# Kernel optimization log

Measured on AMD Instinct MI355X. Metric: run time of the kernel, lower is better.

## Reference

```python
import jax, jax.numpy as jnp
import numpy as np

N, D, NC, K = 4096, 64, 1000, 8192
ALPHA, BETA, GAMMA, SUPT = 0.02, 1.0, 1.0, 1.0
TEMP, BASE_TEMP = 0.05, 0.05
L_INTRA, L_IMEAN, L_IMIN, L_FISHER, EPS = 1.0, 0.1, 0.05, 0.1, 1e-6


def _l2norm(x, axis):
    # torch F.normalize: x / max(||x||, 1e-12)
    n = jnp.sqrt(jnp.sum(x * x, axis=axis, keepdims=True))
    return x / jnp.maximum(n, 1e-12)


def setup_inputs() -> dict:
    key = jax.random.key(0)
    k1, k2, k3, k4, k5 = jax.random.split(key, 5)
    # long-tailed class counts -> log_prior and class_weight buffers
    cls_arr = np.maximum((1280.0 * 0.01 ** (np.arange(NC) / (NC - 1))).astype(np.float32), 1.0)
    prior = cls_arr / cls_arr.sum()
    log_prior = jnp.asarray(np.log(prior), dtype=jnp.float32)
    inv = 1.0 / cls_arr
    class_weight = jnp.asarray((inv / inv.sum() * NC).astype(np.float32))
    feats = jax.random.normal(k1, (N, D), jnp.float32)
    logits = jax.random.normal(k2, (N, NC), jnp.float32)
    labels = jax.random.randint(k3, (N,), 0, NC)
    C = jax.random.normal(k4, (D, NC), jnp.float32) * 0.01  # learnable centers
    queue = jax.random.normal(k5, (K, D), jnp.float32)       # momentum queue buffer
    return {"feats": feats, "logits": logits, "labels": labels, "C": C,
            "queue": queue, "log_prior": log_prior, "class_weight": class_weight}


def reference(feats, logits, labels, C, queue, log_prior, class_weight):
    sg = jax.lax.stop_gradient
    # ---- weighted cross entropy on prior-adjusted logits ----
    sup_logits = (logits + log_prior) / SUPT
    logp = jax.nn.log_softmax(sup_logits, axis=1)
    w = class_weight[labels]
    nll = -jnp.take_along_axis(logp, labels[:, None], axis=1)[:, 0]
    ce_loss = jnp.sum(w * nll) / jnp.sum(w)

    # ---- normalize feats, enqueue (ptr=0, N<=K -> queue[:N] = feats) ----
    f = _l2norm(feats, axis=1)                       # [N, D]
    q = queue.at[:N].set(sg(f))                      # updated queue [K, D]
    centers = _l2norm(C, axis=0).T                   # [NC, D]

    neg_center_sim = f @ centers.T                   # [N, NC]
    neg_queue_sim = f @ q.T                          # [N, K]
    anchor_dot = jnp.concatenate([sg(sup_logits), neg_center_sim, neg_queue_sim], axis=1) / TEMP

    onehot = jax.nn.one_hot(labels, NC, dtype=jnp.float32)  # mask_sup == mask_cent
    mask = jnp.concatenate([onehot * BETA, onehot * ALPHA, jnp.zeros((N, K), jnp.float32)], axis=1)
    logits_mask = jnp.concatenate([jnp.ones((N, 2 * NC), jnp.float32),
                                   jnp.full((N, K), GAMMA, jnp.float32)], axis=1)

    anchor_dot = anchor_dot - sg(jnp.max(anchor_dot, axis=1, keepdims=True))
    exp_logits = jnp.exp(anchor_dot) * logits_mask
    log_prob = anchor_dot - jnp.log(jnp.sum(exp_logits, axis=1, keepdims=True) + 1e-12)
    mean_log_prob_pos = jnp.sum(mask * log_prob, axis=1) / (jnp.sum(mask, axis=1) + 1e-12)
    contrast_loss = -jnp.mean(mean_log_prob_pos) * (TEMP / BASE_TEMP)

    # ---- center regularizers ----
    gram = centers @ centers.T                       # centers are unit-norm rows
    sq = jnp.maximum(2.0 - 2.0 * gram, 1e-12)
    eye = jnp.eye(NC, dtype=bool)
    dist = jnp.sqrt(jnp.where(eye, 1e12, sq))
    dist_no_dg = jnp.where(eye, 1e6, dist)
    inter_min = jnp.min(dist_no_dg)
    inter_mean = jnp.sum(jnp.where(eye, 0.0, dist)) / (NC * (NC - 1))

    diff = f - centers[labels]                       # [N, D]
    intra_d = jnp.mean(jnp.sum(diff * diff, axis=1))
    mu_g = jnp.mean(f, axis=0, keepdims=True)
    cls_cnt = jnp.zeros((NC,), jnp.float32).at[labels].add(1.0)
    S_W = jnp.sum(diff * diff)
    S_B = jnp.sum(jnp.sum((centers - mu_g) ** 2, axis=1) * cls_cnt)
    fisher = S_B / (S_W + EPS)
    reg = (L_INTRA * intra_d + L_IMEAN / (inter_mean + EPS)
           + L_IMIN / (inter_min + EPS) + L_FISHER / (fisher + EPS))
    return ce_loss + contrast_loss + reg
```

## Files before the change

### kernel.cpp

```cpp
#include <hip/hip_runtime.h>
#include <math.h>

#define N_ 4096
#define D_ 64
#define NC_ 1000
#define KQ_ 8192
#define VCOLS 9192
#define VPAD  9216
#define PCH   73
#define TEMP_INV 20.0f
#define M0 20.25f
#define LOG2E 1.4426950408889634f
#define K2L  (TEMP_INV * LOG2E)
#define M0L  (M0 * LOG2E)

#define WS_F     0
#define WS_CENT  (WS_F + N_*D_)
#define WS_SUPM  (WS_CENT + NC_*D_)
#define WS_PSUP  (WS_SUPM + N_)
#define WS_PCENT (WS_PSUP + N_)
#define WS_CEPN  (WS_PCENT + N_)
#define WS_CEPD  (WS_CEPN + 1024)
#define WS_CSP   (WS_CEPD + 1024)
#define WS_GS    (WS_CSP + 16)
#define WS_GM    (WS_GS + 128)
#define WS_VF    (WS_GM + 128)
#define WS_VC    (WS_VF + 4096)
#define WS_TP    (WS_VC + 4096)
#define WS_CTR   (WS_TP + 64)
#define WS_PS    (WS_CTR + 4)
#define WS_BBF   (WS_PS + N_*PCH)

#define K1_BLOCKS 3082
#define K2_BLOCKS 4800
#define K3_BLOCKS 16

typedef __attribute__((ext_vector_type(8))) short short8_t;
typedef __attribute__((ext_vector_type(4))) float f32x4;

__device__ __forceinline__ ushort f2bf(float x) {
    union { float f; unsigned u; } v; v.f = x;
    unsigned r = (v.u + 0x7FFFu + ((v.u >> 16) & 1u)) >> 16;
    return (ushort)r;
}

__global__ __launch_bounds__(256) void k1(const float* __restrict__ feats,
                                          const float* __restrict__ C,
                                          const float* __restrict__ queue,
                                          const float* __restrict__ logits,
                                          const int* __restrict__ labels,
                                          const float* __restrict__ log_prior,
                                          const float* __restrict__ class_weight,
                                          float* __restrict__ ws,
                                          ushort* __restrict__ B) {
    int b = blockIdx.x;
    int t = threadIdx.x;
    if (b == 0 && t == 0) ((unsigned*)ws)[WS_CTR] = 0u;
    if (b < 1024) {
        int row  = b * 4 + (t >> 6);
        int lane = t & 63;
        float x = feats[row * D_ + lane];
        float ss = x * x;
        #pragma unroll
        for (int m = 32; m >= 1; m >>= 1) ss += __shfl_xor(ss, m, 64);
        float y = x / fmaxf(sqrtf(ss), 1e-12f);
        ws[WS_F + row * D_ + lane] = y;
        B[(size_t)(NC_ + row) * D_ + lane] = f2bf(y);
    } else if (b < 1028) {
        int c = (b - 1024) * 256 + t;
        if (c >= NC_) return;
        float v[D_];
        float ss = 0.0f;
        #pragma unroll
        for (int d = 0; d < D_; ++d) { float x = C[d * NC_ + c]; v[d] = x; ss += x * x; }
        float inv = 1.0f / fmaxf(sqrtf(ss), 1e-12f);
        #pragma unroll
        for (int d = 0; d < D_; ++d) {
            float y = v[d] * inv;
            ws[WS_CENT + c * D_ + d] = y;
            B[(size_t)c * D_ + d] = f2bf(y);
        }
    } else if (b < 2058) {
        int q = (b - 1028) * 256 + t;
        if (q >= (KQ_ - N_ + 24) * D_) return;
        int r = q >> 6, d = q & 63;
        ushort o = 0;
        if (r < KQ_ - N_) o = f2bf(queue[(size_t)(N_ + r) * D_ + d]);
        B[(size_t)(NC_ + N_ + r) * D_ + d] = o;
    } else {
        __shared__ float lp[1024];
        __shared__ float cep[4][2];
        int sid = b - 2058;
        if (t < 250) ((float4*)lp)[t] = ((const float4*)log_prior)[t];
        __syncthreads();
        int w = t >> 6, l = t & 63;
        int row = sid * 4 + w;
        const float* lrow = logits + (size_t)row * NC_;
        const float4* lrow4 = (const float4*)lrow;
        float vals[16];
        float m = -1e30f;
        #pragma unroll
        for (int it = 0; it < 4; ++it) {
            int idx = it * 64 + l;
            float4 v4 = (idx < 250) ? lrow4[idx]
                                    : make_float4(-1e30f, -1e30f, -1e30f, -1e30f);
            float4 p4 = (idx < 250) ? ((const float4*)lp)[idx]
                                    : make_float4(0, 0, 0, 0);
            vals[it * 4 + 0] = v4.x + p4.x;
            vals[it * 4 + 1] = v4.y + p4.y;
            vals[it * 4 + 2] = v4.z + p4.z;
            vals[it * 4 + 3] = v4.w + p4.w;
            #pragma unroll
            for (int k = 0; k < 4; ++k) m = fmaxf(m, vals[it * 4 + k]);
        }
        #pragma unroll
        for (int msk = 1; msk < 64; msk <<= 1) m = fmaxf(m, __shfl_xor(m, msk, 64));
        float s1 = 0.0f, s20 = 0.0f;
        #pragma unroll
        for (int k = 0; k < 16; ++k) {
            float d = vals[k] - m;
            s1  += __builtin_amdgcn_exp2f(d * LOG2E);
            s20 += __builtin_amdgcn_exp2f(d * K2L);
        }
        #pragma unroll
        for (int msk = 1; msk < 64; msk <<= 1) {
            s1  += __shfl_xor(s1, msk, 64);
            s20 += __shfl_xor(s20, msk, 64);
        }
        if (l == 0) {
            int lab = labels[row];
            float vpos = lrow[lab] + lp[lab];
            float wt = class_weight[lab];
            cep[w][0] = wt * (m + __logf(s1) - vpos);
            cep[w][1] = wt;
            ws[WS_SUPM + row] = TEMP_INV * m;
            ws[WS_PS + (size_t)row * PCH + (PCH - 1)] = s20;
            ws[WS_PSUP + row] = TEMP_INV * vpos;
        }
        __syncthreads();
        if (t == 0) {
            ws[WS_CEPN + sid] = cep[0][0] + cep[1][0] + cep[2][0] + cep[3][0];
            ws[WS_CEPD + sid] = cep[0][1] + cep[1][1] + cep[2][1] + cep[3][1];
        }
    }
}

__global__ __launch_bounds__(256) void k2(const ushort* __restrict__ B,
                                          const int* __restrict__ labels,
                                          const float* __restrict__ f,
                                          const float* __restrict__ cent,
                                          float* __restrict__ ws) {
    __shared__ ushort At[64 * 64];
    __shared__ ushort Bt[128 * 64];
    __shared__ float ssum[64][2];
    __shared__ float gs4[4], gm4[4];
    __shared__ float svf[4][64], svc[4][64], stp[4];

    int t = threadIdx.x;
    int l = t & 63, w = t >> 6;
    int bid = blockIdx.x;
    int wm = w >> 1, wn = w & 1;
    int lr = l & 15, lg = l >> 4;
    int lk = lg * 8;

    if (bid >= 192) {
        int g = bid - 192;
        int cg = g >> 6;
        int bx = g & 63;
        int r0 = bx * 64;
        int c0 = cg * 128;

        const ushort* Ag = B + (size_t)(NC_ + r0) * D_;
        const ushort* Bg = B + (size_t)c0 * D_;
        #pragma unroll
        for (int i = 0; i < 2; ++i) {
            int cid = t + i * 256;
            *(short8_t*)(At + cid * 8) = *(const short8_t*)(Ag + cid * 8);
        }
        #pragma unroll
        for (int i = 0; i < 4; ++i) {
            int cid = t + i * 256;
            *(short8_t*)(Bt + cid * 8) = *(const short8_t*)(Bg + cid * 8);
        }
        __syncthreads();

        short8_t a[2][2], bfr[4][2];
        #pragma unroll
        for (int rf = 0; rf < 2; ++rf) {
            int row = wm * 32 + rf * 16 + lr;
            #pragma unroll
            for (int ks = 0; ks < 2; ++ks)
                a[rf][ks] = *(const short8_t*)(At + row * D_ + lk + ks * 32);
        }
        #pragma unroll
        for (int cf = 0; cf < 4; ++cf) {
            int col = wn * 64 + cf * 16 + lr;
            #pragma unroll
            for (int ks = 0; ks < 2; ++ks)
                bfr[cf][ks] = *(const short8_t*)(Bt + col * D_ + lk + ks * 32);
        }

        f32x4 acc[2][4] = {};
        #pragma unroll
        for (int ks = 0; ks < 2; ++ks)
            #pragma unroll
            for (int rf = 0; rf < 2; ++rf)
                #pragma unroll
                for (int cf = 0; cf < 4; ++cf)
                    acc[rf][cf] = __builtin_amdgcn_mfma_f32_16x16x32_bf16(
                        a[rf][ks], bfr[cf][ks], acc[rf][cf], 0, 0, 0);

        if (c0 < NC_) {
            #pragma unroll
            for (int rf = 0; rf < 2; ++rf)
                #pragma unroll
                for (int reg = 0; reg < 4; ++reg) {
                    int row = r0 + wm * 32 + rf * 16 + lg * 4 + reg;
                    int lab = labels[row];
                    #pragma unroll
                    for (int cf = 0; cf < 4; ++cf) {
                        int col = c0 + wn * 64 + cf * 16 + lr;
                        if (col == lab) ws[WS_PCENT + row] = acc[rf][cf][reg];
                    }
                }
        }

        #pragma unroll
        for (int rf = 0; rf < 2; ++rf) {
            float se[4] = {0, 0, 0, 0};
            #pragma unroll
            for (int cf = 0; cf < 4; ++cf)
                #pragma unroll
                for (int reg = 0; reg < 4; ++reg)
                    se[reg] += __builtin_amdgcn_exp2f(
                        fmaf(acc[rf][cf][reg], K2L, -M0L));
            #pragma unroll
            for (int reg = 0; reg < 4; ++reg) {
                float v = se[reg];
                #pragma unroll
                for (int msk = 1; msk < 16; msk <<= 1)
                    v += __shfl_xor(v, msk, 64);
                if (lr == 0) ssum[wm * 32 + rf * 16 + lg * 4 + reg][wn] = v;
            }
        }
        __syncthreads();
        if (t < 64)
            ws[WS_PS + (size_t)(r0 + t) * PCH + cg] = ssum[t][0] + ssum[t][1];
    } else if (bid < 128) {
        int g = bid;
        int gr = g >> 3, gc = g & 7;
        int r0 = gr * 64 + wm * 32;
        int c0 = gc * 128 + wn * 64;

        const ushort* Af = B + (size_t)(r0 + lr) * D_ + lk;
        const ushort* Bf = B + (size_t)(c0 + lr) * D_ + lk;

        short8_t a[2][2], bfr[4][2];
        #pragma unroll
        for (int rf = 0; rf < 2; ++rf)
            #pragma unroll
            for (int ks = 0; ks < 2; ++ks)
                a[rf][ks] = *(const short8_t*)(Af + rf * 16 * D_ + ks * 32);
        #pragma unroll
        for (int cf = 0; cf < 4; ++cf)
            #pragma unroll
            for (int ks = 0; ks < 2; ++ks)
                bfr[cf][ks] = *(const short8_t*)(Bf + cf * 16 * D_ + ks * 32);

        f32x4 acc[2][4] = {};
        #pragma unroll
        for (int ks = 0; ks < 2; ++ks)
            #pragma unroll
            for (int rf = 0; rf < 2; ++rf)
                #pragma unroll
                for (int cf = 0; cf < 4; ++cf)
                    acc[rf][cf] = __builtin_amdgcn_mfma_f32_16x16x32_bf16(
                        a[rf][ks], bfr[cf][ks], acc[rf][cf], 0, 0, 0);

        float lsum = 0.0f, lmin = 1e30f;
        #pragma unroll
        for (int rf = 0; rf < 2; ++rf)
            #pragma unroll
            for (int cf = 0; cf < 4; ++cf)
                #pragma unroll
                for (int reg = 0; reg < 4; ++reg) {
                    int gi = r0 + rf * 16 + lg * 4 + reg;
                    int gj = c0 + cf * 16 + lr;
                    if (gi < NC_ && gj < NC_ && gi != gj) {
                        float d = sqrtf(fmaxf(2.0f - 2.0f * acc[rf][cf][reg], 1e-12f));
                        lsum += d;
                        lmin = fminf(lmin, d);
                    }
                }
        #pragma unroll
        for (int msk = 1; msk < 64; msk <<= 1) {
            lsum += __shfl_xor(lsum, msk, 64);
            lmin = fminf(lmin, __shfl_xor(lmin, msk, 64));
        }
        if (l == 0) { gs4[w] = lsum; gm4[w] = lmin; }
        __syncthreads();
        if (t == 0) {
            ws[WS_GS + g] = gs4[0] + gs4[1] + gs4[2] + gs4[3];
            ws[WS_GM + g] = fminf(fminf(gm4[0], gm4[1]), fminf(gm4[2], gm4[3]));
        }
    } else {
        int sb = bid - 128;
        int wid = sb * 4 + w;
        float vf = 0.0f, vc = 0.0f, tacc = 0.0f;
        for (int i = wid; i < N_; i += 256) {
            float x = f[i * D_ + l];
            float c = cent[labels[i] * D_ + l];
            vf += x; vc += c; tacc += x * c;
        }
        #pragma unroll
        for (int msk = 32; msk >= 1; msk >>= 1) tacc += __shfl_xor(tacc, msk, 64);
        svf[w][l] = vf; svc[w][l] = vc;
        if (l == 0) stp[w] = tacc;
        __syncthreads();
        if (w == 0) {
            ws[WS_VF + sb * 64 + l] = svf[0][l] + svf[1][l] + svf[2][l] + svf[3][l];
            ws[WS_VC + sb * 64 + l] = svc[0][l] + svc[1][l] + svc[2][l] + svc[3][l];
            if (l == 0) ws[WS_TP + sb] = stp[0] + stp[1] + stp[2] + stp[3];
        }
    }
}

__global__ __launch_bounds__(256) void k3(float* __restrict__ ws,
                                          float* __restrict__ out) {
    int t = threadIdx.x;
    int w = t >> 6, l = t & 63;
    int bid = blockIdx.x;
    __shared__ unsigned done;
    __shared__ float cb[4];

    {
        int row = bid * 256 + t;
        const float* pv = ws + WS_PS + (size_t)row * PCH;
        float s = 0.0f;
        #pragma unroll
        for (int c = 0; c < PCH - 1; ++c) s += pv[c];
        float msup = ws[WS_SUPM + row];
        float ssup = pv[PCH - 1];
        float M = fmaxf(M0, msup);
        float stot = s * __builtin_amdgcn_exp2f((M0 - M) * LOG2E)
                   + ssup * __builtin_amdgcn_exp2f((msup - M) * LOG2E);
        float logS = __logf(stot + 1e-12f);
        float lp1 = ws[WS_PSUP + row] - M - logS;
        float lp2 = ws[WS_PCENT + row] * TEMP_INV - M - logS;
        float cacc = (lp1 + 0.02f * lp2) / (1.02f + 1e-12f);
        #pragma unroll
        for (int msk = 1; msk < 64; msk <<= 1) cacc += __shfl_xor(cacc, msk, 64);
        if (l == 0) cb[w] = cacc;
        __syncthreads();
        if (t == 0) ws[WS_CSP + bid] = cb[0] + cb[1] + cb[2] + cb[3];
    }

    __threadfence();
    if (t == 0) done = atomicAdd((unsigned*)ws + WS_CTR, 1u);
    __syncthreads();
    if (done != K3_BLOCKS - 1) return;
    __threadfence();

    float csum = (t < 16) ? ws[WS_CSP + t] : 0.0f;
    float cen = 0.0f, ced = 0.0f;
    #pragma unroll
    for (int k = 0; k < 4; ++k) {
        cen += ws[WS_CEPN + t + k * 256];
        ced += ws[WS_CEPD + t + k * 256];
    }
    float gsum = 0, gmin = 1e30f, vf = 0, vc = 0, tp = 0;
    if (t < 64) {
        tp = ws[WS_TP + t];
        #pragma unroll 8
        for (int b = 0; b < 64; ++b) {
            vf += ws[WS_VF + b * 64 + t];
            vc += ws[WS_VC + b * 64 + t];
        }
    }
    if (t < 128) { gsum = ws[WS_GS + t]; gmin = ws[WS_GM + t]; }
    float mu_d = vf * (1.0f / (float)N_);
    float vmu  = vc * mu_d;
    float mumu = mu_d * mu_d;
    #pragma unroll
    for (int m = 32; m >= 1; m >>= 1) {
        csum += __shfl_xor(csum, m, 64);
        cen  += __shfl_xor(cen, m, 64);
        ced  += __shfl_xor(ced, m, 64);
        gsum += __shfl_xor(gsum, m, 64);
        gmin = fminf(gmin, __shfl_xor(gmin, m, 64));
        vmu  += __shfl_xor(vmu, m, 64);
        mumu += __shfl_xor(mumu, m, 64);
        tp   += __shfl_xor(tp, m, 64);
    }
    __shared__ float red[4][8];
    if (l == 0) {
        red[w][0] = csum; red[w][1] = cen; red[w][2] = ced; red[w][3] = gsum;
        red[w][4] = gmin; red[w][5] = vmu; red[w][6] = mumu; red[w][7] = tp;
    }
    __syncthreads();
    if (t == 0) {
        float CSM = red[0][0] + red[1][0] + red[2][0] + red[3][0];
        float CEN = red[0][1] + red[1][1] + red[2][1] + red[3][1];
        float CED = red[0][2] + red[1][2] + red[2][2] + red[3][2];
        float GSM = red[0][3] + red[1][3] + red[2][3] + red[3][3];
        float GMN = fminf(fminf(red[0][4], red[1][4]), fminf(red[2][4], red[3][4]));
        float VMU = red[0][5] + red[1][5] + red[2][5] + red[3][5];
        float MUMU = red[0][6] + red[1][6] + red[2][6] + red[3][6];
        float T   = red[0][7] + red[1][7] + red[2][7] + red[3][7];
        float SW = 2.0f * (float)N_ - 2.0f * T;
        float SB = (float)N_ - 2.0f * VMU + (float)N_ * MUMU;
        float intra = SW / (float)N_;
        float fisher = SB / (SW + 1e-6f);
        float ce = CEN / CED;
        float contrast = -(CSM / (float)N_);
        float inter_mean = GSM / (float)(NC_ * (NC_ - 1));
        float reg = intra + 0.1f / (inter_mean + 1e-6f)
                  + 0.05f / (GMN + 1e-6f) + 0.1f / (fisher + 1e-6f);
        out[0] = ce + contrast + reg;
    }
}

extern "C" void kernel_launch(void* const* d_in, const int* in_sizes, int n_in,
                              void* d_out, int out_size, void* d_ws, size_t ws_size,
                              hipStream_t stream) {
    const float* feats        = (const float*)d_in[0];
    const float* logits       = (const float*)d_in[1];
    const int*   labels       = (const int*)d_in[2];
    const float* C            = (const float*)d_in[3];
    const float* queue        = (const float*)d_in[4];
    const float* log_prior    = (const float*)d_in[5];
    const float* class_weight = (const float*)d_in[6];
    float* ws  = (float*)d_ws;
    float* out = (float*)d_out;
    ushort* Bbf = (ushort*)(ws + WS_BBF);

    hipLaunchKernelGGL(k1, dim3(K1_BLOCKS), dim3(256), 0, stream,
                       feats, C, queue, logits, labels, log_prior, class_weight,
                       ws, Bbf);
    hipLaunchKernelGGL(k2, dim3(K2_BLOCKS), dim3(256), 0, stream,
                       Bbf, labels, ws + WS_F, ws + WS_CENT, ws);
    hipLaunchKernelGGL(k3, dim3(K3_BLOCKS), dim3(256), 0, stream, ws, out);
}
```

Before: 46.26 us.

## Move CE row-softmax into GEMM kernel and swizzle LDS tiles

```diff
diff --git a/kernel.cpp b/kernel.cpp
--- a/kernel.cpp
+++ b/kernel.cpp
@@ -31,8 +31,8 @@
 #define WS_PS    (WS_CTR + 4)
 #define WS_BBF   (WS_PS + N_*PCH)
 
-#define K1_BLOCKS 3082
-#define K2_BLOCKS 4800
+#define K1_BLOCKS 2058
+#define K2_BLOCKS 5824
 #define K3_BLOCKS 16
 
 typedef __attribute__((ext_vector_type(8))) short short8_t;
@@ -44,13 +44,13 @@
     return (ushort)r;
 }
 
+__device__ __forceinline__ int swz(int byte) {
+    return byte ^ (((byte >> 7) & 7) << 4);
+}
+
 __global__ __launch_bounds__(256) void k1(const float* __restrict__ feats,
                                           const float* __restrict__ C,
                                           const float* __restrict__ queue,
-                                          const float* __restrict__ logits,
-                                          const int* __restrict__ labels,
-                                          const float* __restrict__ log_prior,
-                                          const float* __restrict__ class_weight,
                                           float* __restrict__ ws,
                                           ushort* __restrict__ B) {
     int b = blockIdx.x;
@@ -80,21 +80,125 @@
             ws[WS_CENT + c * D_ + d] = y;
             B[(size_t)c * D_ + d] = f2bf(y);
         }
-    } else if (b < 2058) {
+    } else {
         int q = (b - 1028) * 256 + t;
         if (q >= (KQ_ - N_ + 24) * D_) return;
         int r = q >> 6, d = q & 63;
         ushort o = 0;
         if (r < KQ_ - N_) o = f2bf(queue[(size_t)(N_ + r) * D_ + d]);
         B[(size_t)(NC_ + N_ + r) * D_ + d] = o;
-    } else {
-        __shared__ float lp[1024];
-        __shared__ float cep[4][2];
-        int sid = b - 2058;
+    }
+}
+
+__global__ __launch_bounds__(256) void k2(const ushort* __restrict__ B,
+                                          const float* __restrict__ logits,
+                                          const int* __restrict__ labels,
+                                          const float* __restrict__ log_prior,
+                                          const float* __restrict__ class_weight,
+                                          const float* __restrict__ f,
+                                          const float* __restrict__ cent,
+                                          float* __restrict__ ws) {
+    __shared__ char smem[25600];
+    int t = threadIdx.x;
+    int l = t & 63, w = t >> 6;
+    int bid = blockIdx.x;
+    int wm = w >> 1, wn = w & 1;
+    int lr = l & 15, lg = l >> 4;
+    int lk = lg * 8;
+
+    if (bid >= 1216) {
+        char* AtC = smem;
+        char* BtC = smem + 8192;
+        float (*ssum)[2] = (float(*)[2])(smem + 24576);
+
+        int g = bid - 1216;
+        int cg = g >> 6;
+        int bx = g & 63;
+        int r0 = bx * 64;
+        int c0 = cg * 128;
+
+        const short8_t* Ag8 = (const short8_t*)(B + (size_t)(NC_ + r0) * D_);
+        const short8_t* Bg8 = (const short8_t*)(B + (size_t)c0 * D_);
+        #pragma unroll
+        for (int i = 0; i < 2; ++i) {
+            int cid = t + i * 256;
+            *(short8_t*)(AtC + swz(cid * 16)) = Ag8[cid];
+        }
+        #pragma unroll
+        for (int i = 0; i < 4; ++i) {
+            int cid = t + i * 256;
+            *(short8_t*)(BtC + swz(cid * 16)) = Bg8[cid];
+        }
+        __syncthreads();
+
+        short8_t a[2][2], bfr[4][2];
+        #pragma unroll
+        for (int rf = 0; rf < 2; ++rf) {
+            int row = wm * 32 + rf * 16 + lr;
+            #pragma unroll
+            for (int ks = 0; ks < 2; ++ks)
+                a[rf][ks] = *(const short8_t*)(AtC + swz(row * 128 + ks * 64 + lg * 16));
+        }
+        #pragma unroll
+        for (int cf = 0; cf < 4; ++cf) {
+            int col = wn * 64 + cf * 16 + lr;
+            #pragma unroll
+            for (int ks = 0; ks < 2; ++ks)
+                bfr[cf][ks] = *(const short8_t*)(BtC + swz(col * 128 + ks * 64 + lg * 16));
+        }
+
+        f32x4 acc[2][4] = {};
+        #pragma unroll
+        for (int ks = 0; ks < 2; ++ks)
+            #pragma unroll
+            for (int rf = 0; rf < 2; ++rf)
+                #pragma unroll
+                for (int cf = 0; cf < 4; ++cf)
+                    acc[rf][cf] = __builtin_amdgcn_mfma_f32_16x16x32_bf16(
+                        a[rf][ks], bfr[cf][ks], acc[rf][cf], 0, 0, 0);
+
+        if (c0 < NC_) {
+            #pragma unroll
+            for (int rf = 0; rf < 2; ++rf)
+                #pragma unroll
+                for (int reg = 0; reg < 4; ++reg) {
+                    int row = r0 + wm * 32 + rf * 16 + lg * 4 + reg;
+                    int lab = labels[row];
+                    #pragma unroll
+                    for (int cf = 0; cf < 4; ++cf) {
+                        int col = c0 + wn * 64 + cf * 16 + lr;
+                        if (col == lab) ws[WS_PCENT + row] = acc[rf][cf][reg];
+                    }
+                }
+        }
+
+        #pragma unroll
+        for (int rf = 0; rf < 2; ++rf) {
+            float se[4] = {0, 0, 0, 0};
+            #pragma unroll
+            for (int cf = 0; cf < 4; ++cf)
+                #pragma unroll
+                for (int reg = 0; reg < 4; ++reg)
+                    se[reg] += __builtin_amdgcn_exp2f(
+                        fmaf(acc[rf][cf][reg], K2L, -M0L));
+            #pragma unroll
+            for (int reg = 0; reg < 4; ++reg) {
+                float v = se[reg];
+                #pragma unroll
+                for (int msk = 1; msk < 16; msk <<= 1)
+                    v += __shfl_xor(v, msk, 64);
+                if (lr == 0) ssum[wm * 32 + rf * 16 + lg * 4 + reg][wn] = v;
+            }
+        }
+        __syncthreads();
+        if (t < 64)
+            ws[WS_PS + (size_t)(r0 + t) * PCH + cg] = ssum[t][0] + ssum[t][1];
+    } else if (bid < 1024) {
+        float* lp = (float*)smem;
+        float (*cep)[2] = (float(*)[2])(smem + 4096);
         if (t < 250) ((float4*)lp)[t] = ((const float4*)log_prior)[t];
         __syncthreads();
-        int w = t >> 6, l = t & 63;
-        int row = sid * 4 + w;
+        int row = bid * 4 + w;
         const float* lrow = logits + (size_t)row * NC_;
         const float4* lrow4 = (const float4*)lrow;
         float vals[16];
@@ -139,115 +243,13 @@
         }
         __syncthreads();
         if (t == 0) {
-            ws[WS_CEPN + sid] = cep[0][0] + cep[1][0] + cep[2][0] + cep[3][0];
-            ws[WS_CEPD + sid] = cep[0][1] + cep[1][1] + cep[2][1] + cep[3][1];
-        }
-    }
-}
-
-__global__ __launch_bounds__(256) void k2(const ushort* __restrict__ B,
-                                          const int* __restrict__ labels,
-                                          const float* __restrict__ f,
-                                          const float* __restrict__ cent,
-                                          float* __restrict__ ws) {
-    __shared__ ushort At[64 * 64];
-    __shared__ ushort Bt[128 * 64];
-    __shared__ float ssum[64][2];
-    __shared__ float gs4[4], gm4[4];
-    __shared__ float svf[4][64], svc[4][64], stp[4];
-
-    int t = threadIdx.x;
-    int l = t & 63, w = t >> 6;
-    int bid = blockIdx.x;
-    int wm = w >> 1, wn = w & 1;
-    int lr = l & 15, lg = l >> 4;
-    int lk = lg * 8;
-
-    if (bid >= 192) {
-        int g = bid - 192;
-        int cg = g >> 6;
-        int bx = g & 63;
-        int r0 = bx * 64;
-        int c0 = cg * 128;
-
-        const ushort* Ag = B + (size_t)(NC_ + r0) * D_;
-        const ushort* Bg = B + (size_t)c0 * D_;
-        #pragma unroll
-        for (int i = 0; i < 2; ++i) {
-            int cid = t + i * 256;
-            *(short8_t*)(At + cid * 8) = *(const short8_t*)(Ag + cid * 8);
-        }
-        #pragma unroll
-        for (int i = 0; i < 4; ++i) {
-            int cid = t + i * 256;
-            *(short8_t*)(Bt + cid * 8) = *(const short8_t*)(Bg + cid * 8);
-        }
-        __syncthreads();
-
-        short8_t a[2][2], bfr[4][2];
-        #pragma unroll
-        for (int rf = 0; rf < 2; ++rf) {
-            int row = wm * 32 + rf * 16 + lr;
-            #pragma unroll
-            for (int ks = 0; ks < 2; ++ks)
-                a[rf][ks] = *(const short8_t*)(At + row * D_ + lk + ks * 32);
-        }
-        #pragma unroll
-        for (int cf = 0; cf < 4; ++cf) {
-            int col = wn * 64 + cf * 16 + lr;
-            #pragma unroll
-            for (int ks = 0; ks < 2; ++ks)
-                bfr[cf][ks] = *(const short8_t*)(Bt + col * D_ + lk + ks * 32);
-        }
-
-        f32x4 acc[2][4] = {};
-        #pragma unroll
-        for (int ks = 0; ks < 2; ++ks)
-            #pragma unroll
-            for (int rf = 0; rf < 2; ++rf)
-                #pragma unroll
-                for (int cf = 0; cf < 4; ++cf)
-                    acc[rf][cf] = __builtin_amdgcn_mfma_f32_16x16x32_bf16(
-                        a[rf][ks], bfr[cf][ks], acc[rf][cf], 0, 0, 0);
-
-        if (c0 < NC_) {
-            #pragma unroll
-            for (int rf = 0; rf < 2; ++rf)
-                #pragma unroll
-                for (int reg = 0; reg < 4; ++reg) {
-                    int row = r0 + wm * 32 + rf * 16 + lg * 4 + reg;
-                    int lab = labels[row];
-                    #pragma unroll
-                    for (int cf = 0; cf < 4; ++cf) {
-                        int col = c0 + wn * 64 + cf * 16 + lr;
-                        if (col == lab) ws[WS_PCENT + row] = acc[rf][cf][reg];
-                    }
-                }
-        }
-
-        #pragma unroll
-        for (int rf = 0; rf < 2; ++rf) {
-            float se[4] = {0, 0, 0, 0};
-            #pragma unroll
-            for (int cf = 0; cf < 4; ++cf)
-                #pragma unroll
-                for (int reg = 0; reg < 4; ++reg)
-                    se[reg] += __builtin_amdgcn_exp2f(
-                        fmaf(acc[rf][cf][reg], K2L, -M0L));
-            #pragma unroll
-            for (int reg = 0; reg < 4; ++reg) {
-                float v = se[reg];
-                #pragma unroll
-                for (int msk = 1; msk < 16; msk <<= 1)
-                    v += __shfl_xor(v, msk, 64);
-                if (lr == 0) ssum[wm * 32 + rf * 16 + lg * 4 + reg][wn] = v;
-            }
-        }
-        __syncthreads();
-        if (t < 64)
-            ws[WS_PS + (size_t)(r0 + t) * PCH + cg] = ssum[t][0] + ssum[t][1];
-    } else if (bid < 128) {
-        int g = bid;
+            ws[WS_CEPN + bid] = cep[0][0] + cep[1][0] + cep[2][0] + cep[3][0];
+            ws[WS_CEPD + bid] = cep[0][1] + cep[1][1] + cep[2][1] + cep[3][1];
+        }
+    } else if (bid < 1152) {
+        float* gs4 = (float*)smem;
+        float* gm4 = gs4 + 4;
+        int g = bid - 1024;
         int gr = g >> 3, gc = g & 7;
         int r0 = gr * 64 + wm * 32;
         int c0 = gc * 128 + wn * 64;
@@ -304,7 +306,10 @@
             ws[WS_GM + g] = fminf(fminf(gm4[0], gm4[1]), fminf(gm4[2], gm4[3]));
         }
     } else {
-        int sb = bid - 128;
+        float* svf = (float*)smem;
+        float* svc = svf + 256;
+        float* stp = svc + 256;
+        int sb = bid - 1152;
         int wid = sb * 4 + w;
         float vf = 0.0f, vc = 0.0f, tacc = 0.0f;
         for (int i = wid; i < N_; i += 256) {
@@ -314,12 +319,12 @@
         }
         #pragma unroll
         for (int msk = 32; msk >= 1; msk >>= 1) tacc += __shfl_xor(tacc, msk, 64);
-        svf[w][l] = vf; svc[w][l] = vc;
+        svf[w * 64 + l] = vf; svc[w * 64 + l] = vc;
         if (l == 0) stp[w] = tacc;
         __syncthreads();
         if (w == 0) {
-            ws[WS_VF + sb * 64 + l] = svf[0][l] + svf[1][l] + svf[2][l] + svf[3][l];
-            ws[WS_VC + sb * 64 + l] = svc[0][l] + svc[1][l] + svc[2][l] + svc[3][l];
+            ws[WS_VF + sb * 64 + l] = svf[l] + svf[64 + l] + svf[128 + l] + svf[192 + l];
+            ws[WS_VC + sb * 64 + l] = svc[l] + svc[64 + l] + svc[128 + l] + svc[192 + l];
             if (l == 0) ws[WS_TP + sb] = stp[0] + stp[1] + stp[2] + stp[3];
         }
     }
@@ -435,9 +440,9 @@
     ushort* Bbf = (ushort*)(ws + WS_BBF);
 
     hipLaunchKernelGGL(k1, dim3(K1_BLOCKS), dim3(256), 0, stream,
-                       feats, C, queue, logits, labels, log_prior, class_weight,
-                       ws, Bbf);
+                       feats, C, queue, ws, Bbf);
     hipLaunchKernelGGL(k2, dim3(K2_BLOCKS), dim3(256), 0, stream,
-                       Bbf, labels, ws + WS_F, ws + WS_CENT, ws);
+                       Bbf, logits, labels, log_prior, class_weight,
+                       ws + WS_F, ws + WS_CENT, ws);
     hipLaunchKernelGGL(k3, dim3(K3_BLOCKS), dim3(256), 0, stream, ws, out);
 }
```

Result: faster. 43.69 us (-5.6%).
